# Kernel tuning notes

Measured on AMD Instinct MI355X. Metric: run time of the kernel, lower is better.

Reference implementation:

```python
import jax, jax.numpy as jnp
import numpy as np

S, B, NC = 16, 8, 5
D, H, DH = 256, 16, 16
PS, IMG = 7, 28
P = (IMG // PS) ** 2  # 16 patches
L = 2
PD = PS * PS * 1  # 49
EF, EFT = 4, 0.5
DFT = int(EFT * D)


def layernorm(x, g, b, eps=1e-5):
    m = x.mean(-1, keepdims=True)
    v = ((x - m) ** 2).mean(-1, keepdims=True)
    return (x - m) / jnp.sqrt(v + eps) * g + b


def patchify(x):
    # 's b c (h p1) (w p2) -> s b (h w) (p1 p2 c)'
    s, bb, c, hh, ww = x.shape
    h, w = hh // PS, ww // PS
    x = x.reshape(s, bb, c, h, PS, w, PS)
    x = x.transpose(0, 1, 3, 5, 4, 6, 2)
    return x.reshape(s, bb, h * w, PS * PS * c)


def srwm(x, Wy, Wq, Wk, wb, ln_g, ln_b):
    # Stateful self-referential weight matrix layer (Irie et al. 2022).
    # x: (S, Bn, h*dh); Wy/Wq/Wk: (h, dh, dh); wb: (h, 4, dh)
    s, bn, dim = x.shape
    h, dh = Wy.shape[0], Wy.shape[1]
    xs = x.reshape(s, bn, h, dh)
    bc = lambda W: jnp.broadcast_to(W[None], (bn,) + W.shape)

    def step(carry, xt):
        Wy, Wq, Wk, wb = carry
        y = jnp.einsum('bhij,bhj->bhi', Wy, xt)
        q = jnp.einsum('bhij,bhj->bhi', Wq, xt)
        k = jnp.einsum('bhij,bhj->bhi', Wk, xt)
        beta = jax.nn.sigmoid(jnp.einsum('bhcj,bhj->bhc', wb, xt))  # (Bn,h,4)
        qs = jax.nn.softmax(q, -1)
        ks = jax.nn.softmax(k, -1)
        # old values retrieved with k, target values generated with q
        vy_k = jnp.einsum('bhij,bhj->bhi', Wy, ks)
        vq_k = jnp.einsum('bhij,bhj->bhi', Wq, ks)
        vk_k = jnp.einsum('bhij,bhj->bhi', Wk, ks)
        vb_k = jnp.einsum('bhcj,bhj->bhc', wb, ks)
        vy_q = jax.nn.softmax(jnp.einsum('bhij,bhj->bhi', Wy, qs), -1)
        vq_q = jnp.einsum('bhij,bhj->bhi', Wq, qs)
        vk_q = jnp.einsum('bhij,bhj->bhi', Wk, qs)
        vb_q = jnp.einsum('bhcj,bhj->bhc', wb, qs)
        upd = lambda d, bt: bt[..., None, None] * d[..., None] * ks[..., None, :]
        Wy = Wy + upd(vy_q - vy_k, beta[..., 0])
        Wq = Wq + upd(vq_q - vq_k, beta[..., 1])
        Wk = Wk + upd(vk_q - vk_k, beta[..., 2])
        wb = wb + beta[..., 3, None, None] * (vb_q - vb_k)[..., None] * ks[..., None, :]
        return (Wy, Wq, Wk, wb), y

    _, ys = jax.lax.scan(step, (bc(Wy), bc(Wq), bc(Wk), bc(wb)), xs)
    return layernorm(ys.reshape(s, bn, dim), ln_g, ln_b)


def setup_inputs():
    key = jax.random.key(0)
    ks = iter(jax.random.split(key, 64))
    n = lambda shape, sc: jax.random.normal(next(ks), shape, jnp.float32) * sc
    return dict(
        x=jax.random.normal(next(ks), (S, B, 1, IMG, IMG), jnp.float32),
        fb=jax.random.randint(next(ks), (S, B), 0, NC),
        in_W=n((PD + NC, D), (PD + NC) ** -0.5), in_b=jnp.zeros((D,)),
        tk_Wy=n((L, 1, P, P), P ** -0.5), tk_Wq=n((L, 1, P, P), 0.01 * P ** -0.5),
        tk_Wk=n((L, 1, P, P), P ** -0.5), tk_wb=n((L, 1, 4, P), P ** -0.5),
        tk_lng=jnp.ones((L, P)), tk_lnb=jnp.zeros((L, P)),
        tkm_g=jnp.ones((L, D)), tkm_b=jnp.zeros((L, D)),
        tkm_W1=n((L, P, EF * P), P ** -0.5), tkm_b1=jnp.zeros((L, EF * P)),
        tkm_W2=n((L, EF * P, P), (EF * P) ** -0.5), tkm_b2=jnp.zeros((L, P)),
        ch_Wy=n((L, H, DH, DH), DH ** -0.5), ch_Wq=n((L, H, DH, DH), 0.01 * DH ** -0.5),
        ch_Wk=n((L, H, DH, DH), DH ** -0.5), ch_wb=n((L, H, 4, DH), DH ** -0.5),
        ch_lng=jnp.ones((L, D)), ch_lnb=jnp.zeros((L, D)),
        chm_g=jnp.ones((L, D)), chm_b=jnp.zeros((L, D)),
        chm_W1=n((L, D, DFT), D ** -0.5), chm_b1=jnp.zeros((L, DFT)),
        chm_W2=n((L, DFT, D), DFT ** -0.5), chm_b2=jnp.zeros((L, D)),
        fln_g=jnp.ones((D,)), fln_b=jnp.zeros((D,)),
        o_Wy=n((H, DH, DH), DH ** -0.5), o_Wq=n((H, DH, DH), 0.01 * DH ** -0.5),
        o_Wk=n((H, DH, DH), DH ** -0.5), o_wb=n((H, 4, DH), DH ** -0.5),
        o_lng=jnp.ones((D,)), o_lnb=jnp.zeros((D,)),
        out_W=n((D, NC), D ** -0.5), out_b=jnp.zeros((NC,)),
    )


def reference(x, fb, in_W, in_b, tk_Wy, tk_Wq, tk_Wk, tk_wb, tk_lng, tk_lnb,
              tkm_g, tkm_b, tkm_W1, tkm_b1, tkm_W2, tkm_b2,
              ch_Wy, ch_Wq, ch_Wk, ch_wb, ch_lng, ch_lnb,
              chm_g, chm_b, chm_W1, chm_b1, chm_W2, chm_b2,
              fln_g, fln_b, o_Wy, o_Wq, o_Wk, o_wb, o_lng, o_lnb, out_W, out_b):
    xp = patchify(x)  # (S,B,P,PD)
    emb = jnp.broadcast_to(jax.nn.one_hot(fb, NC)[:, :, None, :], (S, B, P, NC))
    h = jnp.concatenate([xp, emb.astype(xp.dtype)], -1) @ in_W + in_b  # (S,B,P,D)
    for i in range(L):
        # token SRWM: features = patch axis, batch = B*D
        t = jnp.swapaxes(h, -2, -1).reshape(S, B * D, P)
        t = srwm(t, tk_Wy[i], tk_Wq[i], tk_Wk[i], tk_wb[i], tk_lng[i], tk_lnb[i])
        h = jnp.swapaxes(t.reshape(S, B, D, P), -2, -1)
        # token mixer (pre-norm residual, FFN over patch axis)
        hn = jnp.swapaxes(layernorm(h, tkm_g[i], tkm_b[i]), -2, -1)
        hn = jax.nn.gelu(hn @ tkm_W1[i] + tkm_b1[i]) @ tkm_W2[i] + tkm_b2[i]
        h = h + jnp.swapaxes(hn, -2, -1)
        # channel SRWM: features = hidden axis, batch = B*P
        c = srwm(h.reshape(S, B * P, D), ch_Wy[i], ch_Wq[i], ch_Wk[i], ch_wb[i], ch_lng[i], ch_lnb[i])
        h = c.reshape(S, B, P, D)
        # channel mixer
        hn = layernorm(h, chm_g[i], chm_b[i])
        h = h + (jax.nn.gelu(hn @ chm_W1[i] + chm_b1[i]) @ chm_W2[i] + chm_b2[i])
    h = layernorm(h, fln_g, fln_b).mean(-2)  # (S,B,D) mean over patches
    h = srwm(h, o_Wy, o_Wq, o_Wk, o_wb, o_lng, o_lnb)
    return h @ out_W + out_b  # (S,B,NC)
```

## Files before the change

### kernel.cpp

```cpp
#include <hip/hip_runtime.h>
#include <math.h>

constexpr int cS  = 16;
constexpr int cB  = 8;
constexpr int cNC = 5;
constexpr int cD  = 256;
constexpr int cP  = 16;
constexpr int cPD = 49;
#define LEPS 1e-5f

__device__ __forceinline__ float frcp(float x) { return __builtin_amdgcn_rcpf(x); }
__device__ __forceinline__ float sigm(float x) { return frcp(1.0f + __expf(-x)); }
__device__ __forceinline__ float gelu_t(float x) {
  const float z = 1.5957691216057308f * (x + 0.044715f * x * x * x);
  return x * frcp(1.0f + __expf(-z));
}

template<int CTRL>
__device__ __forceinline__ float dpp_mov(float v) {
  return __int_as_float(__builtin_amdgcn_update_dpp(
      0, __float_as_int(v), CTRL, 0xF, 0xF, true));
}
__device__ __forceinline__ float row_sum16(float v) {
  v += dpp_mov<0xB1>(v);
  v += dpp_mov<0x4E>(v);
  v += dpp_mov<0x124>(v);
  v += dpp_mov<0x128>(v);
  return v;
}
__device__ __forceinline__ float wave_sum64(float v) {
  v = row_sum16(v);
  v += __shfl_xor(v, 16, 64);
  v += __shfl_xor(v, 32, 64);
  return v;
}

__device__ __forceinline__ float dot16(const float (&w)[16],
    const float4 a, const float4 b, const float4 c, const float4 d) {
  float s0 = w[0]  * a.x; s0 += w[1]  * a.y; s0 += w[2]  * a.z; s0 += w[3]  * a.w;
  float s1 = w[4]  * b.x; s1 += w[5]  * b.y; s1 += w[6]  * b.z; s1 += w[7]  * b.w;
  float s2 = w[8]  * c.x; s2 += w[9]  * c.y; s2 += w[10] * c.z; s2 += w[11] * c.w;
  float s3 = w[12] * d.x; s3 += w[13] * d.y; s3 += w[14] * d.z; s3 += w[15] * d.w;
  return (s0 + s1) + (s2 + s3);
}

__device__ __forceinline__ float srwm_step(
    float xv, float (&wy)[16], float (&wq)[16], float (&wk)[16], float (&wbr)[16],
    float* gl, const int r) {
  gl[r] = xv;
  __builtin_amdgcn_wave_barrier();
  const float4* g4 = (const float4*)gl;
  const float4 xa = g4[0], xb = g4[1], xc = g4[2], xd = g4[3];
  const float y  = dot16(wy,  xa, xb, xc, xd);
  const float q  = dot16(wq,  xa, xb, xc, xd);
  const float k  = dot16(wk,  xa, xb, xc, xd);
  const float bt = dot16(wbr, xa, xb, xc, xd);
  const float bsig = sigm(bt);
  const float eq = __expf(q), ek = __expf(k);
  gl[16 + r] = eq;
  gl[32 + r] = ek;
  gl[48 + r] = bsig;
  __builtin_amdgcn_wave_barrier();
  const float4 qa = g4[4], qb = g4[5], qc = g4[6],  qd = g4[7];
  const float4 ka = g4[8], kb = g4[9], kc = g4[10], kd = g4[11];
  const float4 bs4 = g4[12];
  const float ay  = dot16(wy,  qa, qb, qc, qd);
  const float vqq = dot16(wq,  qa, qb, qc, qd);
  const float vkq = dot16(wk,  qa, qb, qc, qd);
  const float vbq = dot16(wbr, qa, qb, qc, qd);
  const float vyk = dot16(wy,  ka, kb, kc, kd);
  const float vqk = dot16(wq,  ka, kb, kc, kd);
  const float vkk = dot16(wk,  ka, kb, kc, kd);
  const float vbk = dot16(wbr, ka, kb, kc, kd);
  const float sq = ((qa.x + qa.y) + (qa.z + qa.w)) + ((qb.x + qb.y) + (qb.z + qb.w))
                 + ((qc.x + qc.y) + (qc.z + qc.w)) + ((qd.x + qd.y) + (qd.z + qd.w));
  const float sk = ((ka.x + ka.y) + (ka.z + ka.w)) + ((kb.x + kb.y) + (kb.z + kb.w))
                 + ((kc.x + kc.y) + (kc.z + kc.w)) + ((kd.x + kd.y) + (kd.z + kd.w));
  const float rq = frcp(sq);
  const float rk = frcp(sk);
  const float ea = __expf(ay * rq);
  const float vyq = ea * frcp(row_sum16(ea));
  const float cy = bs4.x * (vyq      - vyk * rk) * rk;
  const float cq = bs4.y * (vqq * rq - vqk * rk) * rk;
  const float ck = bs4.z * (vkq * rq - vkk * rk) * rk;
  const float cb = bs4.w * (vbq * rq - vbk * rk) * rk;
  const float ks[16] = {ka.x, ka.y, ka.z, ka.w, kb.x, kb.y, kb.z, kb.w,
                        kc.x, kc.y, kc.z, kc.w, kd.x, kd.y, kd.z, kd.w};
#pragma unroll
  for (int j = 0; j < 16; ++j) {
    wy[j] += cy * ks[j]; wq[j] += cq * ks[j]; wk[j] += ck * ks[j]; wbr[j] += cb * ks[j];
  }
  return y;
}

__global__ __launch_bounds__(256) void k_embed(const float* __restrict__ x,
                                               const int* __restrict__ fb,
                                               const float* __restrict__ inW,
                                               const float* __restrict__ inb,
                                               float* __restrict__ h) {
  const int blk = blockIdx.x;
  const int p  = blk & 15;
  const int sb = blk >> 4;
  const int ph = p >> 2, pw = p & 3;
  __shared__ float sx[cPD];
  const int t = threadIdx.x;
  if (t < cPD) {
    const int p1 = t / 7, p2 = t % 7;
    sx[t] = x[(size_t)sb * 784 + (ph * 7 + p1) * 28 + (pw * 7 + p2)];
  }
  __syncthreads();
  const int cls = fb[sb];
  float acc = inb[t] + inW[(size_t)(cPD + cls) * cD + t];
#pragma unroll
  for (int j = 0; j < cPD; ++j) acc += sx[j] * inW[(size_t)j * cD + t];
  h[((size_t)sb * cP + p) * cD + t] = acc;
}

__global__ __launch_bounds__(128) void k_tok_srwm(
    float* __restrict__ h, const float* __restrict__ Wy0, const float* __restrict__ Wq0,
    const float* __restrict__ Wk0, const float* __restrict__ wb0,
    const float* __restrict__ lng, const float* __restrict__ lnb) {
  const int t    = threadIdx.x;
  const int lane = t & 63;
  const int w    = t >> 6;
  const int r    = lane & 15;
  const int li   = lane >> 4;
  const int b    = blockIdx.x >> 5;
  const int d    = ((blockIdx.x & 31) << 3) + (w << 2) + li;
  __shared__ __align__(16) float gscr[8][64];
  float* gl = gscr[t >> 4];
  float wy[16], wq[16], wk[16], wbr[16];
#pragma unroll
  for (int j = 0; j < 16; ++j) {
    wy[j]  = Wy0[r * 16 + j];
    wq[j]  = Wq0[r * 16 + j];
    wk[j]  = Wk0[r * 16 + j];
    wbr[j] = wb0[(r & 3) * 16 + j];
  }
  const float gg = lng[r], bb = lnb[r];
  float xp[16];
#pragma unroll
  for (int s = 0; s < 16; ++s)
    xp[s] = h[((size_t)(s * cB + b) * cP + r) * cD + d];
  for (int s = 0; s < cS; ++s) {
    const float y = srwm_step(xp[s], wy, wq, wk, wbr, gl, r);
    const float s1 = row_sum16(y);
    const float s2 = row_sum16(y * y);
    const float m = s1 * 0.0625f;
    const float var = s2 * 0.0625f - m * m;
    h[((size_t)(s * cB + b) * cP + r) * cD + d] = (y - m) * rsqrtf(var + LEPS) * gg + bb;
  }
}

__global__ __launch_bounds__(256) void k_tok_mixer(
    float* __restrict__ h, const float* __restrict__ g, const float* __restrict__ bta,
    const float* __restrict__ W1, const float* __restrict__ b1,
    const float* __restrict__ W2, const float* __restrict__ b2) {
  const int sb = blockIdx.x;
  const int t = threadIdx.x;
  __shared__ float tile[16][256];
  __shared__ float W1s[16 * 64], W2s[64 * 16];
  __shared__ float mean_[16], rstd_[16];
  __shared__ float red[16][17], red2[16][17];
  const size_t base = (size_t)sb * cP * cD;
#pragma unroll
  for (int p = 0; p < 16; ++p) tile[p][t] = h[base + p * 256 + t];
  W1s[t] = W1[t]; W1s[t + 256] = W1[t + 256]; W1s[t + 512] = W1[t + 512]; W1s[t + 768] = W1[t + 768];
  W2s[t] = W2[t]; W2s[t + 256] = W2[t + 256]; W2s[t + 512] = W2[t + 512]; W2s[t + 768] = W2[t + 768];
  __syncthreads();
  const int p = t >> 4, l = t & 15;
  float ps = 0.f, ps2 = 0.f;
#pragma unroll
  for (int k = 0; k < 16; ++k) { const float v = tile[p][l + 16 * k]; ps += v; ps2 += v * v; }
  red[p][l] = ps; red2[p][l] = ps2;
  __syncthreads();
  if (t < 16) {
    float sm = 0.f, s2 = 0.f;
#pragma unroll
    for (int k = 0; k < 16; ++k) { sm += red[t][k]; s2 += red2[t][k]; }
    const float m = sm * (1.f / 256.f);
    mean_[t] = m;
    rstd_[t] = rsqrtf(s2 * (1.f / 256.f) - m * m + LEPS);
  }
  __syncthreads();
  const float gd = g[t], bd = bta[t];
  float v[16], out[16];
#pragma unroll
  for (int pp = 0; pp < 16; ++pp) {
    v[pp] = (tile[pp][t] - mean_[pp]) * rstd_[pp] * gd + bd;
    out[pp] = b2[pp];
  }
  for (int e = 0; e < 64; ++e) {
    float acc = b1[e];
#pragma unroll
    for (int pp = 0; pp < 16; ++pp) acc += v[pp] * W1s[pp * 64 + e];
    const float ge = gelu_t(acc);
#pragma unroll
    for (int pp = 0; pp < 16; ++pp) out[pp] += ge * W2s[e * 16 + pp];
  }
#pragma unroll
  for (int pp = 0; pp < 16; ++pp) h[base + pp * 256 + t] = tile[pp][t] + out[pp];
}

__global__ __launch_bounds__(128) void k_ch_scan(
    const float* __restrict__ h, float* __restrict__ y2,
    const float* __restrict__ Wy0, const float* __restrict__ Wq0,
    const float* __restrict__ Wk0, const float* __restrict__ wb0) {
  const int t  = threadIdx.x;
  const int hg = blockIdx.x & 1;
  const int bp = blockIdx.x >> 1;
  const int hh = (hg << 3) + (t >> 4);
  const int r  = t & 15;
  const int d  = (hg << 7) + t;
  __shared__ __align__(16) float gscr[8][64];
  float* gl = gscr[t >> 4];
  float wy[16], wq[16], wk[16], wbr[16];
#pragma unroll
  for (int j = 0; j < 16; ++j) {
    wy[j]  = Wy0[(hh * 16 + r) * 16 + j];
    wq[j]  = Wq0[(hh * 16 + r) * 16 + j];
    wk[j]  = Wk0[(hh * 16 + r) * 16 + j];
    wbr[j] = wb0[(hh * 4 + (r & 3)) * 16 + j];
  }
  float xp[16];
#pragma unroll
  for (int s = 0; s < 16; ++s)
    xp[s] = h[(size_t)(s * cB * cP + bp) * cD + d];
  for (int s = 0; s < cS; ++s)
    y2[(size_t)(s * cB * cP + bp) * cD + d] = srwm_step(xp[s], wy, wq, wk, wbr, gl, r);
}

__global__ __launch_bounds__(256) void k_ch_ln_mix(
    const float* __restrict__ y2, float* __restrict__ h,
    const float* __restrict__ lng, const float* __restrict__ lnb,
    const float* __restrict__ mg, const float* __restrict__ mb,
    const float* __restrict__ W1, const float* __restrict__ b1,
    const float* __restrict__ W2, const float* __restrict__ b2) {
  const int t = threadIdx.x;
  const int row0 = blockIdx.x * 8;
  __shared__ float yv[8][256];
  __shared__ float lnv[8][256];
  __shared__ float hid[8][128];
  const float4* yp4 = (const float4*)(y2 + (size_t)row0 * cD);
  ((float4*)yv)[t]       = yp4[t];
  ((float4*)yv)[t + 256] = yp4[t + 256];
  __syncthreads();
  const int r32 = t >> 5, l = t & 31;
  const float4 eg0 = ((const float4*)lng)[l * 2];
  const float4 eg1 = ((const float4*)lng)[l * 2 + 1];
  const float4 eb0 = ((const float4*)lnb)[l * 2];
  const float4 eb1 = ((const float4*)lnb)[l * 2 + 1];
  const float4 mg0 = ((const float4*)mg)[l * 2];
  const float4 mg1 = ((const float4*)mg)[l * 2 + 1];
  const float4 mb0 = ((const float4*)mb)[l * 2];
  const float4 mb1 = ((const float4*)mb)[l * 2 + 1];
  const float4 y0 = ((const float4*)yv[r32])[l * 2];
  const float4 y1 = ((const float4*)yv[r32])[l * 2 + 1];
  float s1 = y0.x + y0.y + y0.z + y0.w + y1.x + y1.y + y1.z + y1.w;
  float s2 = y0.x * y0.x + y0.y * y0.y + y0.z * y0.z + y0.w * y0.w +
             y1.x * y1.x + y1.y * y1.y + y1.z * y1.z + y1.w * y1.w;
#pragma unroll
  for (int o = 1; o < 32; o <<= 1) {
    s1 += __shfl_xor(s1, o, 32);
    s2 += __shfl_xor(s2, o, 32);
  }
  const float m1 = s1 * (1.f / 256.f);
  const float rst1 = rsqrtf(s2 * (1.f / 256.f) - m1 * m1 + LEPS);
  float4 a0, a1;
  a0.x = (y0.x - m1) * rst1 * eg0.x + eb0.x; a0.y = (y0.y - m1) * rst1 * eg0.y + eb0.y;
  a0.z = (y0.z - m1) * rst1 * eg0.z + eb0.z; a0.w = (y0.w - m1) * rst1 * eg0.w + eb0.w;
  a1.x = (y1.x - m1) * rst1 * eg1.x + eb1.x; a1.y = (y1.y - m1) * rst1 * eg1.y + eb1.y;
  a1.z = (y1.z - m1) * rst1 * eg1.z + eb1.z; a1.w = (y1.w - m1) * rst1 * eg1.w + eb1.w;
  float u1 = a0.x + a0.y + a0.z + a0.w + a1.x + a1.y + a1.z + a1.w;
  float u2 = a0.x * a0.x + a0.y * a0.y + a0.z * a0.z + a0.w * a0.w +
             a1.x * a1.x + a1.y * a1.y + a1.z * a1.z + a1.w * a1.w;
#pragma unroll
  for (int o = 1; o < 32; o <<= 1) {
    u1 += __shfl_xor(u1, o, 32);
    u2 += __shfl_xor(u2, o, 32);
  }
  const float m2 = u1 * (1.f / 256.f);
  const float rst2 = rsqrtf(u2 * (1.f / 256.f) - m2 * m2 + LEPS);
  float4 L0, L1;
  L0.x = (a0.x - m2) * rst2 * mg0.x + mb0.x; L0.y = (a0.y - m2) * rst2 * mg0.y + mb0.y;
  L0.z = (a0.z - m2) * rst2 * mg0.z + mb0.z; L0.w = (a0.w - m2) * rst2 * mg0.w + mb0.w;
  L1.x = (a1.x - m2) * rst2 * mg1.x + mb1.x; L1.y = (a1.y - m2) * rst2 * mg1.y + mb1.y;
  L1.z = (a1.z - m2) * rst2 * mg1.z + mb1.z; L1.w = (a1.w - m2) * rst2 * mg1.w + mb1.w;
  ((float4*)lnv[r32])[l * 2]     = L0;
  ((float4*)lnv[r32])[l * 2 + 1] = L1;
  __syncthreads();
  {
    const float4* W1f = (const float4*)W1;
    float4 acc = ((const float4*)b1)[l];
    for (int j = 0; j < 256; ++j) {
      const float xj = lnv[r32][j];
      const float4 wv = W1f[j * 32 + l];
      acc.x += xj * wv.x; acc.y += xj * wv.y; acc.z += xj * wv.z; acc.w += xj * wv.w;
    }
    float4 hv;
    hv.x = gelu_t(acc.x); hv.y = gelu_t(acc.y);
    hv.z = gelu_t(acc.z); hv.w = gelu_t(acc.w);
    ((float4*)hid[r32])[l] = hv;
  }
  __syncthreads();
  {
    const float4* W2f = (const float4*)W2;
    float4 o0 = ((const float4*)b2)[l * 2];
    float4 o1 = ((const float4*)b2)[l * 2 + 1];
    for (int e = 0; e < 128; ++e) {
      const float xh = hid[r32][e];
      const float4 w0 = W2f[e * 64 + l * 2];
      const float4 w1 = W2f[e * 64 + l * 2 + 1];
      o0.x += xh * w0.x; o0.y += xh * w0.y; o0.z += xh * w0.z; o0.w += xh * w0.w;
      o1.x += xh * w1.x; o1.y += xh * w1.y; o1.z += xh * w1.z; o1.w += xh * w1.w;
    }
    o0.x += a0.x; o0.y += a0.y; o0.z += a0.z; o0.w += a0.w;
    o1.x += a1.x; o1.y += a1.y; o1.z += a1.z; o1.w += a1.w;
    float4* op = (float4*)(h + ((size_t)row0 + r32) * cD);
    op[l * 2]     = o0;
    op[l * 2 + 1] = o1;
  }
}

__global__ __launch_bounds__(256) void k_fln_mean(
    const float* __restrict__ h, const float* __restrict__ gg, const float* __restrict__ bbv,
    float* __restrict__ o) {
  const int sb = blockIdx.x;
  const int t = threadIdx.x;
  const int lane = t & 63, w = t >> 6;
  const float4 g4 = ((const float4*)gg)[lane];
  const float4 b4 = ((const float4*)bbv)[lane];
  float a0 = 0.f, a1 = 0.f, a2 = 0.f, a3 = 0.f;
  for (int pp = 0; pp < 4; ++pp) {
    const int p = w * 4 + pp;
    const float4 v4 = ((const float4*)(h + ((size_t)sb * cP + p) * cD))[lane];
    const float s1 = wave_sum64(v4.x + v4.y + v4.z + v4.w);
    const float s2 = wave_sum64(v4.x * v4.x + v4.y * v4.y + v4.z * v4.z + v4.w * v4.w);
    const float m = s1 * (1.f / 256.f);
    const float rst = rsqrtf(s2 * (1.f / 256.f) - m * m + LEPS);
    a0 += (v4.x - m) * rst * g4.x + b4.x;
    a1 += (v4.y - m) * rst * g4.y + b4.y;
    a2 += (v4.z - m) * rst * g4.z + b4.z;
    a3 += (v4.w - m) * rst * g4.w + b4.w;
  }
  __shared__ float sacc[4][256];
  float4* sp = (float4*)sacc[w];
  sp[lane] = make_float4(a0, a1, a2, a3);
  __syncthreads();
  o[(size_t)sb * cD + t] = (sacc[0][t] + sacc[1][t] + sacc[2][t] + sacc[3][t]) * (1.f / 16.f);
}

__global__ __launch_bounds__(256, 1) void k_out_srwm(
    const float* __restrict__ gin, float* __restrict__ outp,
    const float* __restrict__ Wy0, const float* __restrict__ Wq0,
    const float* __restrict__ Wk0, const float* __restrict__ wb0,
    const float* __restrict__ lng, const float* __restrict__ lnb,
    const float* __restrict__ outW, const float* __restrict__ outb) {
  const int t = threadIdx.x;
  const int lane = t & 63;
  const int w = t >> 6;
  const int hh = t >> 4, r = t & 15;
  const int b = blockIdx.x;
  __shared__ float ymat[16][256];
  __shared__ float gwm[cNC][256];
  __shared__ float GBp[4][10];
  __shared__ float GBs[10];
  __shared__ __align__(16) float gscr[16][64];
  float* gl = gscr[hh];
  float wy[16], wq[16], wk[16], wbr[16];
#pragma unroll
  for (int j = 0; j < 16; ++j) {
    wy[j]  = Wy0[(hh * 16 + r) * 16 + j];
    wq[j]  = Wq0[(hh * 16 + r) * 16 + j];
    wk[j]  = Wk0[(hh * 16 + r) * 16 + j];
    wbr[j] = wb0[(hh * 4 + (r & 3)) * 16 + j];
  }
  {
    const float gg = lng[t], bbl = lnb[t];
    float pg[cNC], pbv[cNC];
#pragma unroll
    for (int c = 0; c < cNC; ++c) {
      const float wv = outW[(size_t)t * cNC + c];
      const float gwv = gg * wv;
      gwm[c][t] = gwv;
      pg[c] = wave_sum64(gwv);
      pbv[c] = wave_sum64(bbl * wv);
    }
    if (lane == 0) {
#pragma unroll
      for (int c = 0; c < cNC; ++c) { GBp[w][c] = pg[c]; GBp[w][5 + c] = pbv[c]; }
    }
    __syncthreads();
    if (t < 10) GBs[t] = GBp[0][t] + GBp[1][t] + GBp[2][t] + GBp[3][t];
    __syncthreads();
  }
  float xp[16];
#pragma unroll
  for (int s = 0; s < 16; ++s) xp[s] = gin[(size_t)(s * cB + b) * cD + t];
  for (int s = 0; s < cS; ++s)
    ymat[s][t] = srwm_step(xp[s], wy, wq, wk, wbr, gl, r);
  __syncthreads();
  for (int k2 = 0; k2 < 4; ++k2) {
    const int sidx = w * 4 + k2;
    const float4 y4 = ((const float4*)ymat[sidx])[lane];
    const float s1 = wave_sum64(y4.x + y4.y + y4.z + y4.w);
    const float s2 = wave_sum64(y4.x * y4.x + y4.y * y4.y + y4.z * y4.z + y4.w * y4.w);
    float S[cNC];
#pragma unroll
    for (int c = 0; c < cNC; ++c) {
      const float4 g4 = ((const float4*)gwm[c])[lane];
      S[c] = wave_sum64(y4.x * g4.x + y4.y * g4.y + y4.z * g4.z + y4.w * g4.w);
    }
    if (lane == 0) {
      const float m = s1 * (1.f / 256.f);
      const float var = s2 * (1.f / 256.f) - m * m;
      const float rst = rsqrtf(var + LEPS);
#pragma unroll
      for (int c = 0; c < cNC; ++c) {
        outp[(size_t)(sidx * cB + b) * cNC + c] =
            outb[c] + rst * S[c] - rst * m * GBs[c] + GBs[5 + c];
      }
    }
  }
}

extern "C" void kernel_launch(void* const* d_in, const int* in_sizes, int n_in,
                              void* d_out, int out_size, void* d_ws, size_t ws_size,
                              hipStream_t stream) {
  const float* x     = (const float*)d_in[0];
  const int*   fb    = (const int*)d_in[1];
  const float* inW   = (const float*)d_in[2];
  const float* inb   = (const float*)d_in[3];
  const float* tkWy  = (const float*)d_in[4];
  const float* tkWq  = (const float*)d_in[5];
  const float* tkWk  = (const float*)d_in[6];
  const float* tkwb  = (const float*)d_in[7];
  const float* tklng = (const float*)d_in[8];
  const float* tklnb = (const float*)d_in[9];
  const float* tkmg  = (const float*)d_in[10];
  const float* tkmb  = (const float*)d_in[11];
  const float* tkmW1 = (const float*)d_in[12];
  const float* tkmb1 = (const float*)d_in[13];
  const float* tkmW2 = (const float*)d_in[14];
  const float* tkmb2 = (const float*)d_in[15];
  const float* chWy  = (const float*)d_in[16];
  const float* chWq  = (const float*)d_in[17];
  const float* chWk  = (const float*)d_in[18];
  const float* chwb  = (const float*)d_in[19];
  const float* chlng = (const float*)d_in[20];
  const float* chlnb = (const float*)d_in[21];
  const float* chmg  = (const float*)d_in[22];
  const float* chmb  = (const float*)d_in[23];
  const float* chmW1 = (const float*)d_in[24];
  const float* chmb1 = (const float*)d_in[25];
  const float* chmW2 = (const float*)d_in[26];
  const float* chmb2 = (const float*)d_in[27];
  const float* flng  = (const float*)d_in[28];
  const float* flnb  = (const float*)d_in[29];
  const float* oWy   = (const float*)d_in[30];
  const float* oWq   = (const float*)d_in[31];
  const float* oWk   = (const float*)d_in[32];
  const float* owb   = (const float*)d_in[33];
  const float* olng  = (const float*)d_in[34];
  const float* olnb  = (const float*)d_in[35];
  const float* outW  = (const float*)d_in[36];
  const float* outb  = (const float*)d_in[37];

  float* h    = (float*)d_ws;
  float* gbuf = h + (size_t)cS * cB * cP * cD;
  float* y2   = gbuf + (size_t)cS * cB * cD;
  float* outp = (float*)d_out;

  k_embed<<<dim3(cS * cB * cP), dim3(256), 0, stream>>>(x, fb, inW, inb, h);
  for (int i = 0; i < 2; ++i) {
    k_tok_srwm<<<dim3(256), dim3(128), 0, stream>>>(
        h, tkWy + i * 256, tkWq + i * 256, tkWk + i * 256, tkwb + i * 64,
        tklng + i * 16, tklnb + i * 16);
    k_tok_mixer<<<dim3(cS * cB), dim3(256), 0, stream>>>(
        h, tkmg + i * 256, tkmb + i * 256, tkmW1 + i * 1024, tkmb1 + i * 64,
        tkmW2 + i * 1024, tkmb2 + i * 16);
    k_ch_scan<<<dim3(cB * cP * 2), dim3(128), 0, stream>>>(
        h, y2, chWy + i * 4096, chWq + i * 4096, chWk + i * 4096, chwb + i * 1024);
    k_ch_ln_mix<<<dim3(cS * cB * cP / 8), dim3(256), 0, stream>>>(
        y2, h, chlng + i * 256, chlnb + i * 256,
        chmg + i * 256, chmb + i * 256, chmW1 + i * 32768, chmb1 + i * 128,
        chmW2 + i * 32768, chmb2 + i * 256);
  }
  k_fln_mean<<<dim3(cS * cB), dim3(256), 0, stream>>>(h, flng, flnb, gbuf);
  k_out_srwm<<<dim3(cB), dim3(256), 0, stream>>>(
      gbuf, outp, oWy, oWq, oWk, owb, olng, olnb, outW, outb);
}
```

Before: 300.4 us.

## Fuse all stages into one persistent kernel with software grid barriers

Replaces the sequence of about ten kernel launches with a single persistent kernel of 256 blocks that runs every stage and separates them with a sense-reversing atomic grid barrier. The embed stage is also reorganised so each block computes eight patches from the full image held in shared memory. The aim is to remove per-launch overhead and inter-kernel gaps, since each stage is small. In exchange, the SRWM stages now leave half the threads idle in 256-thread blocks, several stages use only a subset of blocks, and correctness depends on all 256 blocks being co-resident.

```diff
diff --git a/kernel.cpp b/kernel.cpp
--- a/kernel.cpp
+++ b/kernel.cpp
@@ -8,6 +8,10 @@
 constexpr int cP  = 16;
 constexpr int cPD = 49;
 #define LEPS 1e-5f
+#define NBLK 256
+
+__device__ unsigned g_cnt[2];
+__device__ unsigned g_sense;
 
 __device__ __forceinline__ float frcp(float x) { return __builtin_amdgcn_rcpf(x); }
 __device__ __forceinline__ float sigm(float x) { return frcp(1.0f + __expf(-x)); }
@@ -93,332 +97,397 @@
   return y;
 }
 
-__global__ __launch_bounds__(256) void k_embed(const float* __restrict__ x,
-                                               const int* __restrict__ fb,
-                                               const float* __restrict__ inW,
-                                               const float* __restrict__ inb,
-                                               float* __restrict__ h) {
-  const int blk = blockIdx.x;
-  const int p  = blk & 15;
-  const int sb = blk >> 4;
-  const int ph = p >> 2, pw = p & 3;
-  __shared__ float sx[cPD];
+struct SM_M {
+  float tile[16][256];
+  float W1s[1024]; float W2s[1024];
+  float mean_[16]; float rstd_[16];
+  float red[16][17]; float red2[16][17];
+};
+struct SM_X { float yv[8][256]; float lnv[8][256]; float hid[8][128]; };
+struct SM_O {
+  float ymat[16][256]; float gwm[cNC][256];
+  float GBp[4][10]; float GBs[10]; float gscr[16][64];
+};
+union SMem {
+  float sx[784];
+  float gscr[8][64];
+  SM_M m;
+  SM_X x;
+  float sacc[4][256];
+  SM_O o;
+};
+
+struct Args {
+  const float* x; const int* fb; const float* inW; const float* inb;
+  const float *tkWy, *tkWq, *tkWk, *tkwb, *tklng, *tklnb;
+  const float *tkmg, *tkmb, *tkmW1, *tkmb1, *tkmW2, *tkmb2;
+  const float *chWy, *chWq, *chWk, *chwb, *chlng, *chlnb;
+  const float *chmg, *chmb, *chmW1, *chmb1, *chmW2, *chmb2;
+  const float *flng, *flnb;
+  const float *oWy, *oWq, *oWk, *owb, *olng, *olnb, *outW, *outb;
+  float *h, *gbuf, *y2, *outp;
+};
+
+#define GSYNC()                                                                \
+  do {                                                                         \
+    __syncthreads();                                                           \
+    ++kbar;                                                                    \
+    if (t == 0) {                                                              \
+      __threadfence();                                                         \
+      const unsigned tgt = kbar & 1u;                                          \
+      const unsigned old = __hip_atomic_fetch_add(                             \
+          &g_cnt[kbar & 1u], 1u, __ATOMIC_ACQ_REL, __HIP_MEMORY_SCOPE_AGENT);  \
+      if (old == (unsigned)(NBLK - 1)) {                                       \
+        __hip_atomic_store(&g_cnt[kbar & 1u], 0u, __ATOMIC_RELAXED,            \
+                           __HIP_MEMORY_SCOPE_AGENT);                          \
+        __hip_atomic_store(&g_sense, tgt, __ATOMIC_RELEASE,                    \
+                           __HIP_MEMORY_SCOPE_AGENT);                          \
+      } else {                                                                 \
+        while (__hip_atomic_load(&g_sense, __ATOMIC_ACQUIRE,                   \
+                                 __HIP_MEMORY_SCOPE_AGENT) != tgt)             \
+          __builtin_amdgcn_s_sleep(16);                                        \
+      }                                                                        \
+    }                                                                          \
+    __syncthreads();                                                           \
+  } while (0)
+
+__global__ __launch_bounds__(256, 1) void k_mega(Args a) {
   const int t = threadIdx.x;
-  if (t < cPD) {
-    const int p1 = t / 7, p2 = t % 7;
-    sx[t] = x[(size_t)sb * 784 + (ph * 7 + p1) * 28 + (pw * 7 + p2)];
+  const int bid = blockIdx.x;
+  __shared__ __align__(16) SMem sm;
+  unsigned kbar = 0;
+
+  {
+    const int sb = bid >> 1, h2 = bid & 1;
+    for (int i = t; i < 784; i += 256) sm.sx[i] = a.x[(size_t)sb * 784 + i];
+    __syncthreads();
+    const int cls = a.fb[sb];
+    const int d = t;
+    float acc[8];
+    const float base0 = a.inb[d] + a.inW[(size_t)(cPD + cls) * cD + d];
+#pragma unroll
+    for (int p8 = 0; p8 < 8; ++p8) acc[p8] = base0;
+    for (int p1 = 0; p1 < 7; ++p1) {
+      for (int p2 = 0; p2 < 7; ++p2) {
+        const float wj = a.inW[(size_t)(p1 * 7 + p2) * cD + d];
+        const int jo = p1 * 28 + p2;
+#pragma unroll
+        for (int p8 = 0; p8 < 8; ++p8) {
+          const int p = h2 * 8 + p8;
+          acc[p8] += wj * sm.sx[(p >> 2) * 196 + (p & 3) * 7 + jo];
+        }
+      }
+    }
+#pragma unroll
+    for (int p8 = 0; p8 < 8; ++p8)
+      a.h[((size_t)sb * cP + h2 * 8 + p8) * cD + d] = acc[p8];
   }
-  __syncthreads();
-  const int cls = fb[sb];
-  float acc = inb[t] + inW[(size_t)(cPD + cls) * cD + t];
-#pragma unroll
-  for (int j = 0; j < cPD; ++j) acc += sx[j] * inW[(size_t)j * cD + t];
-  h[((size_t)sb * cP + p) * cD + t] = acc;
-}
-
-__global__ __launch_bounds__(128) void k_tok_srwm(
-    float* __restrict__ h, const float* __restrict__ Wy0, const float* __restrict__ Wq0,
-    const float* __restrict__ Wk0, const float* __restrict__ wb0,
-    const float* __restrict__ lng, const float* __restrict__ lnb) {
-  const int t    = threadIdx.x;
-  const int lane = t & 63;
-  const int w    = t >> 6;
-  const int r    = lane & 15;
-  const int li   = lane >> 4;
-  const int b    = blockIdx.x >> 5;
-  const int d    = ((blockIdx.x & 31) << 3) + (w << 2) + li;
-  __shared__ __align__(16) float gscr[8][64];
-  float* gl = gscr[t >> 4];
-  float wy[16], wq[16], wk[16], wbr[16];
-#pragma unroll
-  for (int j = 0; j < 16; ++j) {
-    wy[j]  = Wy0[r * 16 + j];
-    wq[j]  = Wq0[r * 16 + j];
-    wk[j]  = Wk0[r * 16 + j];
-    wbr[j] = wb0[(r & 3) * 16 + j];
+  GSYNC();
+
+  for (int i = 0; i < 2; ++i) {
+    {
+      const float* Wy0 = a.tkWy + i * 256;
+      const float* Wq0 = a.tkWq + i * 256;
+      const float* Wk0 = a.tkWk + i * 256;
+      const float* wb0 = a.tkwb + i * 64;
+      const float* lng = a.tklng + i * 16;
+      const float* lnb = a.tklnb + i * 16;
+      if (t < 128) {
+        const int lane = t & 63;
+        const int w    = t >> 6;
+        const int r    = lane & 15;
+        const int li   = lane >> 4;
+        const int b    = bid >> 5;
+        const int d    = ((bid & 31) << 3) + (w << 2) + li;
+        float* gl = sm.gscr[t >> 4];
+        float wy[16], wq[16], wk[16], wbr[16];
+#pragma unroll
+        for (int j = 0; j < 16; ++j) {
+          wy[j]  = Wy0[r * 16 + j];
+          wq[j]  = Wq0[r * 16 + j];
+          wk[j]  = Wk0[r * 16 + j];
+          wbr[j] = wb0[(r & 3) * 16 + j];
+        }
+        const float gg = lng[r], bb = lnb[r];
+        float xp[16];
+#pragma unroll
+        for (int s = 0; s < 16; ++s)
+          xp[s] = a.h[((size_t)(s * cB + b) * cP + r) * cD + d];
+        for (int s = 0; s < cS; ++s) {
+          const float y = srwm_step(xp[s], wy, wq, wk, wbr, gl, r);
+          const float s1 = row_sum16(y);
+          const float s2 = row_sum16(y * y);
+          const float m = s1 * 0.0625f;
+          const float var = s2 * 0.0625f - m * m;
+          a.h[((size_t)(s * cB + b) * cP + r) * cD + d] =
+              (y - m) * rsqrtf(var + LEPS) * gg + bb;
+        }
+      }
+    }
+    GSYNC();
+
+    if (bid < 128) {
+      const float* g   = a.tkmg + i * 256;
+      const float* bta = a.tkmb + i * 256;
+      const float* W1  = a.tkmW1 + i * 1024;
+      const float* b1  = a.tkmb1 + i * 64;
+      const float* W2  = a.tkmW2 + i * 1024;
+      const float* b2  = a.tkmb2 + i * 16;
+      const size_t base = (size_t)bid * cP * cD;
+#pragma unroll
+      for (int p = 0; p < 16; ++p) sm.m.tile[p][t] = a.h[base + p * 256 + t];
+      sm.m.W1s[t] = W1[t]; sm.m.W1s[t + 256] = W1[t + 256];
+      sm.m.W1s[t + 512] = W1[t + 512]; sm.m.W1s[t + 768] = W1[t + 768];
+      sm.m.W2s[t] = W2[t]; sm.m.W2s[t + 256] = W2[t + 256];
+      sm.m.W2s[t + 512] = W2[t + 512]; sm.m.W2s[t + 768] = W2[t + 768];
+      __syncthreads();
+      const int p = t >> 4, l = t & 15;
+      float ps = 0.f, ps2 = 0.f;
+#pragma unroll
+      for (int k = 0; k < 16; ++k) {
+        const float v = sm.m.tile[p][l + 16 * k]; ps += v; ps2 += v * v;
+      }
+      sm.m.red[p][l] = ps; sm.m.red2[p][l] = ps2;
+      __syncthreads();
+      if (t < 16) {
+        float smv = 0.f, s2 = 0.f;
+#pragma unroll
+        for (int k = 0; k < 16; ++k) { smv += sm.m.red[t][k]; s2 += sm.m.red2[t][k]; }
+        const float m = smv * (1.f / 256.f);
+        sm.m.mean_[t] = m;
+        sm.m.rstd_[t] = rsqrtf(s2 * (1.f / 256.f) - m * m + LEPS);
+      }
+      __syncthreads();
+      const float gd = g[t], bd = bta[t];
+      float v[16], out[16];
+#pragma unroll
+      for (int pp = 0; pp < 16; ++pp) {
+        v[pp] = (sm.m.tile[pp][t] - sm.m.mean_[pp]) * sm.m.rstd_[pp] * gd + bd;
+        out[pp] = b2[pp];
+      }
+      for (int e = 0; e < 64; ++e) {
+        float acc = b1[e];
+#pragma unroll
+        for (int pp = 0; pp < 16; ++pp) acc += v[pp] * sm.m.W1s[pp * 64 + e];
+        const float ge = gelu_t(acc);
+#pragma unroll
+        for (int pp = 0; pp < 16; ++pp) out[pp] += ge * sm.m.W2s[e * 16 + pp];
+      }
+#pragma unroll
+      for (int pp = 0; pp < 16; ++pp)
+        a.h[base + pp * 256 + t] = sm.m.tile[pp][t] + out[pp];
+    }
+    GSYNC();
+
+    {
+      const float* Wy0 = a.chWy + i * 4096;
+      const float* Wq0 = a.chWq + i * 4096;
+      const float* Wk0 = a.chWk + i * 4096;
+      const float* wb0 = a.chwb + i * 1024;
+      if (t < 128) {
+        const int hg = bid & 1;
+        const int bp = bid >> 1;
+        const int hh = (hg << 3) + (t >> 4);
+        const int r  = t & 15;
+        const int d  = (hg << 7) + t;
+        float* gl = sm.gscr[t >> 4];
+        float wy[16], wq[16], wk[16], wbr[16];
+#pragma unroll
+        for (int j = 0; j < 16; ++j) {
+          wy[j]  = Wy0[(hh * 16 + r) * 16 + j];
+          wq[j]  = Wq0[(hh * 16 + r) * 16 + j];
+          wk[j]  = Wk0[(hh * 16 + r) * 16 + j];
+          wbr[j] = wb0[(hh * 4 + (r & 3)) * 16 + j];
+        }
+        float xp[16];
+#pragma unroll
+        for (int s = 0; s < 16; ++s)
+          xp[s] = a.h[(size_t)(s * cB * cP + bp) * cD + d];
+        for (int s = 0; s < cS; ++s)
+          a.y2[(size_t)(s * cB * cP + bp) * cD + d] =
+              srwm_step(xp[s], wy, wq, wk, wbr, gl, r);
+      }
+    }
+    GSYNC();
+
+    {
+      const float* lng = a.chlng + i * 256;
+      const float* lnb = a.chlnb + i * 256;
+      const float* mg  = a.chmg + i * 256;
+      const float* mb  = a.chmb + i * 256;
+      const float* W1  = a.chmW1 + i * 32768;
+      const float* b1  = a.chmb1 + i * 128;
+      const float* W2  = a.chmW2 + i * 32768;
+      const float* b2  = a.chmb2 + i * 256;
+      const int row0 = bid * 8;
+      const float4* yp4 = (const float4*)(a.y2 + (size_t)row0 * cD);
+      ((float4*)sm.x.yv)[t]       = yp4[t];
+      ((float4*)sm.x.yv)[t + 256] = yp4[t + 256];
+      __syncthreads();
+      const int r32 = t >> 5, l = t & 31;
+      const float4 eg0 = ((const float4*)lng)[l * 2];
+      const float4 eg1 = ((const float4*)lng)[l * 2 + 1];
+      const float4 eb0 = ((const float4*)lnb)[l * 2];
+      const float4 eb1 = ((const float4*)lnb)[l * 2 + 1];
+      const float4 mg0 = ((const float4*)mg)[l * 2];
+      const float4 mg1 = ((const float4*)mg)[l * 2 + 1];
+      const float4 mb0 = ((const float4*)mb)[l * 2];
+      const float4 mb1 = ((const float4*)mb)[l * 2 + 1];
+      const float4 y0 = ((const float4*)sm.x.yv[r32])[l * 2];
+      const float4 y1 = ((const float4*)sm.x.yv[r32])[l * 2 + 1];
+      float s1 = y0.x + y0.y + y0.z + y0.w + y1.x + y1.y + y1.z + y1.w;
+      float s2 = y0.x * y0.x + y0.y * y0.y + y0.z * y0.z + y0.w * y0.w +
+                 y1.x * y1.x + y1.y * y1.y + y1.z * y1.z + y1.w * y1.w;
+#pragma unroll
+      for (int o = 1; o < 32; o <<= 1) {
+        s1 += __shfl_xor(s1, o, 32);
+        s2 += __shfl_xor(s2, o, 32);
+      }
+      const float m1 = s1 * (1.f / 256.f);
+      const float rst1 = rsqrtf(s2 * (1.f / 256.f) - m1 * m1 + LEPS);
+      float4 a0, a1;
+      a0.x = (y0.x - m1) * rst1 * eg0.x + eb0.x; a0.y = (y0.y - m1) * rst1 * eg0.y + eb0.y;
+      a0.z = (y0.z - m1) * rst1 * eg0.z + eb0.z; a0.w = (y0.w - m1) * rst1 * eg0.w + eb0.w;
+      a1.x = (y1.x - m1) * rst1 * eg1.x + eb1.x; a1.y = (y1.y - m1) * rst1 * eg1.y + eb1.y;
+      a1.z = (y1.z - m1) * rst1 * eg1.z + eb1.z; a1.w = (y1.w - m1) * rst1 * eg1.w + eb1.w;
+      float u1 = a0.x + a0.y + a0.z + a0.w + a1.x + a1.y + a1.z + a1.w;
+      float u2 = a0.x * a0.x + a0.y * a0.y + a0.z * a0.z + a0.w * a0.w +
+                 a1.x * a1.x + a1.y * a1.y + a1.z * a1.z + a1.w * a1.w;
+#pragma unroll
+      for (int o = 1; o < 32; o <<= 1) {
+        u1 += __shfl_xor(u1, o, 32);
+        u2 += __shfl_xor(u2, o, 32);
+      }
+      const float m2 = u1 * (1.f / 256.f);
+      const float rst2 = rsqrtf(u2 * (1.f / 256.f) - m2 * m2 + LEPS);
+      float4 L0, L1;
+      L0.x = (a0.x - m2) * rst2 * mg0.x + mb0.x; L0.y = (a0.y - m2) * rst2 * mg0.y + mb0.y;
+      L0.z = (a0.z - m2) * rst2 * mg0.z + mb0.z; L0.w = (a0.w - m2) * rst2 * mg0.w + mb0.w;
+      L1.x = (a1.x - m2) * rst2 * mg1.x + mb1.x; L1.y = (a1.y - m2) * rst2 * mg1.y + mb1.y;
+      L1.z = (a1.z - m2) * rst2 * mg1.z + mb1.z; L1.w = (a1.w - m2) * rst2 * mg1.w + mb1.w;
+      ((float4*)sm.x.lnv[r32])[l * 2]     = L0;
+      ((float4*)sm.x.lnv[r32])[l * 2 + 1] = L1;
+      __syncthreads();
+      {
+        const float4* W1f = (const float4*)W1;
+        float4 acc = ((const float4*)b1)[l];
+        for (int j = 0; j < 256; ++j) {
+          const float xj = sm.x.lnv[r32][j];
+          const float4 wv = W1f[j * 32 + l];
+          acc.x += xj * wv.x; acc.y += xj * wv.y; acc.z += xj * wv.z; acc.w += xj * wv.w;
+        }
+        float4 hv;
+        hv.x = gelu_t(acc.x); hv.y = gelu_t(acc.y);
+        hv.z = gelu_t(acc.z); hv.w = gelu_t(acc.w);
+        ((float4*)sm.x.hid[r32])[l] = hv;
+      }
+      __syncthreads();
+      {
+        const float4* W2f = (const float4*)W2;
+        float4 o0 = ((const float4*)b2)[l * 2];
+        float4 o1 = ((const float4*)b2)[l * 2 + 1];
+        for (int e = 0; e < 128; ++e) {
+          const float xh = sm.x.hid[r32][e];
+          const float4 w0 = W2f[e * 64 + l * 2];
+          const float4 w1 = W2f[e * 64 + l * 2 + 1];
+          o0.x += xh * w0.x; o0.y += xh * w0.y; o0.z += xh * w0.z; o0.w += xh * w0.w;
+          o1.x += xh * w1.x; o1.y += xh * w1.y; o1.z += xh * w1.z; o1.w += xh * w1.w;
+        }
+        o0.x += a0.x; o0.y += a0.y; o0.z += a0.z; o0.w += a0.w;
+        o1.x += a1.x; o1.y += a1.y; o1.z += a1.z; o1.w += a1.w;
+        float4* op = (float4*)(a.h + ((size_t)row0 + r32) * cD);
+        op[l * 2]     = o0;
+        op[l * 2 + 1] = o1;
+      }
+    }
+    GSYNC();
   }
-  const float gg = lng[r], bb = lnb[r];
-  float xp[16];
-#pragma unroll
-  for (int s = 0; s < 16; ++s)
-    xp[s] = h[((size_t)(s * cB + b) * cP + r) * cD + d];
-  for (int s = 0; s < cS; ++s) {
-    const float y = srwm_step(xp[s], wy, wq, wk, wbr, gl, r);
-    const float s1 = row_sum16(y);
-    const float s2 = row_sum16(y * y);
-    const float m = s1 * 0.0625f;
-    const float var = s2 * 0.0625f - m * m;
-    h[((size_t)(s * cB + b) * cP + r) * cD + d] = (y - m) * rsqrtf(var + LEPS) * gg + bb;
+
+  if (bid < 128) {
+    const int sb = bid;
+    const int lane = t & 63, w = t >> 6;
+    const float4 g4 = ((const float4*)a.flng)[lane];
+    const float4 b4 = ((const float4*)a.flnb)[lane];
+    float a0 = 0.f, a1 = 0.f, a2 = 0.f, a3 = 0.f;
+    for (int pp = 0; pp < 4; ++pp) {
+      const int p = w * 4 + pp;
+      const float4 v4 = ((const float4*)(a.h + ((size_t)sb * cP + p) * cD))[lane];
+      const float s1 = wave_sum64(v4.x + v4.y + v4.z + v4.w);
+      const float s2 = wave_sum64(v4.x * v4.x + v4.y * v4.y + v4.z * v4.z + v4.w * v4.w);
+      const float m = s1 * (1.f / 256.f);
+      const float rst = rsqrtf(s2 * (1.f / 256.f) - m * m + LEPS);
+      a0 += (v4.x - m) * rst * g4.x + b4.x;
+      a1 += (v4.y - m) * rst * g4.y + b4.y;
+      a2 += (v4.z - m) * rst * g4.z + b4.z;
+      a3 += (v4.w - m) * rst * g4.w + b4.w;
+    }
+    float4* sp = (float4*)sm.sacc[w];
+    sp[lane] = make_float4(a0, a1, a2, a3);
+    __syncthreads();
+    a.gbuf[(size_t)sb * cD + t] =
+        (sm.sacc[0][t] + sm.sacc[1][t] + sm.sacc[2][t] + sm.sacc[3][t]) * (1.f / 16.f);
   }
-}
-
-__global__ __launch_bounds__(256) void k_tok_mixer(
-    float* __restrict__ h, const float* __restrict__ g, const float* __restrict__ bta,
-    const float* __restrict__ W1, const float* __restrict__ b1,
-    const float* __restrict__ W2, const float* __restrict__ b2) {
-  const int sb = blockIdx.x;
-  const int t = threadIdx.x;
-  __shared__ float tile[16][256];
-  __shared__ float W1s[16 * 64], W2s[64 * 16];
-  __shared__ float mean_[16], rstd_[16];
-  __shared__ float red[16][17], red2[16][17];
-  const size_t base = (size_t)sb * cP * cD;
-#pragma unroll
-  for (int p = 0; p < 16; ++p) tile[p][t] = h[base + p * 256 + t];
-  W1s[t] = W1[t]; W1s[t + 256] = W1[t + 256]; W1s[t + 512] = W1[t + 512]; W1s[t + 768] = W1[t + 768];
-  W2s[t] = W2[t]; W2s[t + 256] = W2[t + 256]; W2s[t + 512] = W2[t + 512]; W2s[t + 768] = W2[t + 768];
-  __syncthreads();
-  const int p = t >> 4, l = t & 15;
-  float ps = 0.f, ps2 = 0.f;
-#pragma unroll
-  for (int k = 0; k < 16; ++k) { const float v = tile[p][l + 16 * k]; ps += v; ps2 += v * v; }
-  red[p][l] = ps; red2[p][l] = ps2;
-  __syncthreads();
-  if (t < 16) {
-    float sm = 0.f, s2 = 0.f;
-#pragma unroll
-    for (int k = 0; k < 16; ++k) { sm += red[t][k]; s2 += red2[t][k]; }
-    const float m = sm * (1.f / 256.f);
-    mean_[t] = m;
-    rstd_[t] = rsqrtf(s2 * (1.f / 256.f) - m * m + LEPS);
-  }
-  __syncthreads();
-  const float gd = g[t], bd = bta[t];
-  float v[16], out[16];
-#pragma unroll
-  for (int pp = 0; pp < 16; ++pp) {
-    v[pp] = (tile[pp][t] - mean_[pp]) * rstd_[pp] * gd + bd;
-    out[pp] = b2[pp];
-  }
-  for (int e = 0; e < 64; ++e) {
-    float acc = b1[e];
-#pragma unroll
-    for (int pp = 0; pp < 16; ++pp) acc += v[pp] * W1s[pp * 64 + e];
-    const float ge = gelu_t(acc);
-#pragma unroll
-    for (int pp = 0; pp < 16; ++pp) out[pp] += ge * W2s[e * 16 + pp];
-  }
-#pragma unroll
-  for (int pp = 0; pp < 16; ++pp) h[base + pp * 256 + t] = tile[pp][t] + out[pp];
-}
-
-__global__ __launch_bounds__(128) void k_ch_scan(
-    const float* __restrict__ h, float* __restrict__ y2,
-    const float* __restrict__ Wy0, const float* __restrict__ Wq0,
-    const float* __restrict__ Wk0, const float* __restrict__ wb0) {
-  const int t  = threadIdx.x;
-  const int hg = blockIdx.x & 1;
-  const int bp = blockIdx.x >> 1;
-  const int hh = (hg << 3) + (t >> 4);
-  const int r  = t & 15;
-  const int d  = (hg << 7) + t;
-  __shared__ __align__(16) float gscr[8][64];
-  float* gl = gscr[t >> 4];
-  float wy[16], wq[16], wk[16], wbr[16];
-#pragma unroll
-  for (int j = 0; j < 16; ++j) {
-    wy[j]  = Wy0[(hh * 16 + r) * 16 + j];
-    wq[j]  = Wq0[(hh * 16 + r) * 16 + j];
-    wk[j]  = Wk0[(hh * 16 + r) * 16 + j];
-    wbr[j] = wb0[(hh * 4 + (r & 3)) * 16 + j];
-  }
-  float xp[16];
-#pragma unroll
-  for (int s = 0; s < 16; ++s)
-    xp[s] = h[(size_t)(s * cB * cP + bp) * cD + d];
-  for (int s = 0; s < cS; ++s)
-    y2[(size_t)(s * cB * cP + bp) * cD + d] = srwm_step(xp[s], wy, wq, wk, wbr, gl, r);
-}
-
-__global__ __launch_bounds__(256) void k_ch_ln_mix(
-    const float* __restrict__ y2, float* __restrict__ h,
-    const float* __restrict__ lng, const float* __restrict__ lnb,
-    const float* __restrict__ mg, const float* __restrict__ mb,
-    const float* __restrict__ W1, const float* __restrict__ b1,
-    const float* __restrict__ W2, const float* __restrict__ b2) {
-  const int t = threadIdx.x;
-  const int row0 = blockIdx.x * 8;
-  __shared__ float yv[8][256];
-  __shared__ float lnv[8][256];
-  __shared__ float hid[8][128];
-  const float4* yp4 = (const float4*)(y2 + (size_t)row0 * cD);
-  ((float4*)yv)[t]       = yp4[t];
-  ((float4*)yv)[t + 256] = yp4[t + 256];
-  __syncthreads();
-  const int r32 = t >> 5, l = t & 31;
-  const float4 eg0 = ((const float4*)lng)[l * 2];
-  const float4 eg1 = ((const float4*)lng)[l * 2 + 1];
-  const float4 eb0 = ((const float4*)lnb)[l * 2];
-  const float4 eb1 = ((const float4*)lnb)[l * 2 + 1];
-  const float4 mg0 = ((const float4*)mg)[l * 2];
-  const float4 mg1 = ((const float4*)mg)[l * 2 + 1];
-  const float4 mb0 = ((const float4*)mb)[l * 2];
-  const float4 mb1 = ((const float4*)mb)[l * 2 + 1];
-  const float4 y0 = ((const float4*)yv[r32])[l * 2];
-  const float4 y1 = ((const float4*)yv[r32])[l * 2 + 1];
-  float s1 = y0.x + y0.y + y0.z + y0.w + y1.x + y1.y + y1.z + y1.w;
-  float s2 = y0.x * y0.x + y0.y * y0.y + y0.z * y0.z + y0.w * y0.w +
-             y1.x * y1.x + y1.y * y1.y + y1.z * y1.z + y1.w * y1.w;
-#pragma unroll
-  for (int o = 1; o < 32; o <<= 1) {
-    s1 += __shfl_xor(s1, o, 32);
-    s2 += __shfl_xor(s2, o, 32);
-  }
-  const float m1 = s1 * (1.f / 256.f);
-  const float rst1 = rsqrtf(s2 * (1.f / 256.f) - m1 * m1 + LEPS);
-  float4 a0, a1;
-  a0.x = (y0.x - m1) * rst1 * eg0.x + eb0.x; a0.y = (y0.y - m1) * rst1 * eg0.y + eb0.y;
-  a0.z = (y0.z - m1) * rst1 * eg0.z + eb0.z; a0.w = (y0.w - m1) * rst1 * eg0.w + eb0.w;
-  a1.x = (y1.x - m1) * rst1 * eg1.x + eb1.x; a1.y = (y1.y - m1) * rst1 * eg1.y + eb1.y;
-  a1.z = (y1.z - m1) * rst1 * eg1.z + eb1.z; a1.w = (y1.w - m1) * rst1 * eg1.w + eb1.w;
-  float u1 = a0.x + a0.y + a0.z + a0.w + a1.x + a1.y + a1.z + a1.w;
-  float u2 = a0.x * a0.x + a0.y * a0.y + a0.z * a0.z + a0.w * a0.w +
-             a1.x * a1.x + a1.y * a1.y + a1.z * a1.z + a1.w * a1.w;
-#pragma unroll
-  for (int o = 1; o < 32; o <<= 1) {
-    u1 += __shfl_xor(u1, o, 32);
-    u2 += __shfl_xor(u2, o, 32);
-  }
-  const float m2 = u1 * (1.f / 256.f);
-  const float rst2 = rsqrtf(u2 * (1.f / 256.f) - m2 * m2 + LEPS);
-  float4 L0, L1;
-  L0.x = (a0.x - m2) * rst2 * mg0.x + mb0.x; L0.y = (a0.y - m2) * rst2 * mg0.y + mb0.y;
-  L0.z = (a0.z - m2) * rst2 * mg0.z + mb0.z; L0.w = (a0.w - m2) * rst2 * mg0.w + mb0.w;
-  L1.x = (a1.x - m2) * rst2 * mg1.x + mb1.x; L1.y = (a1.y - m2) * rst2 * mg1.y + mb1.y;
-  L1.z = (a1.z - m2) * rst2 * mg1.z + mb1.z; L1.w = (a1.w - m2) * rst2 * mg1.w + mb1.w;
-  ((float4*)lnv[r32])[l * 2]     = L0;
-  ((float4*)lnv[r32])[l * 2 + 1] = L1;
-  __syncthreads();
-  {
-    const float4* W1f = (const float4*)W1;
-    float4 acc = ((const float4*)b1)[l];
-    for (int j = 0; j < 256; ++j) {
-      const float xj = lnv[r32][j];
-      const float4 wv = W1f[j * 32 + l];
-      acc.x += xj * wv.x; acc.y += xj * wv.y; acc.z += xj * wv.z; acc.w += xj * wv.w;
-    }
-    float4 hv;
-    hv.x = gelu_t(acc.x); hv.y = gelu_t(acc.y);
-    hv.z = gelu_t(acc.z); hv.w = gelu_t(acc.w);
-    ((float4*)hid[r32])[l] = hv;
-  }
-  __syncthreads();
-  {
-    const float4* W2f = (const float4*)W2;
-    float4 o0 = ((const float4*)b2)[l * 2];
-    float4 o1 = ((const float4*)b2)[l * 2 + 1];
-    for (int e = 0; e < 128; ++e) {
-      const float xh = hid[r32][e];
-      const float4 w0 = W2f[e * 64 + l * 2];
-      const float4 w1 = W2f[e * 64 + l * 2 + 1];
-      o0.x += xh * w0.x; o0.y += xh * w0.y; o0.z += xh * w0.z; o0.w += xh * w0.w;
-      o1.x += xh * w1.x; o1.y += xh * w1.y; o1.z += xh * w1.z; o1.w += xh * w1.w;
-    }
-    o0.x += a0.x; o0.y += a0.y; o0.z += a0.z; o0.w += a0.w;
-    o1.x += a1.x; o1.y += a1.y; o1.z += a1.z; o1.w += a1.w;
-    float4* op = (float4*)(h + ((size_t)row0 + r32) * cD);
-    op[l * 2]     = o0;
-    op[l * 2 + 1] = o1;
-  }
-}
-
-__global__ __launch_bounds__(256) void k_fln_mean(
-    const float* __restrict__ h, const float* __restrict__ gg, const float* __restrict__ bbv,
-    float* __restrict__ o) {
-  const int sb = blockIdx.x;
-  const int t = threadIdx.x;
-  const int lane = t & 63, w = t >> 6;
-  const float4 g4 = ((const float4*)gg)[lane];
-  const float4 b4 = ((const float4*)bbv)[lane];
-  float a0 = 0.f, a1 = 0.f, a2 = 0.f, a3 = 0.f;
-  for (int pp = 0; pp < 4; ++pp) {
-    const int p = w * 4 + pp;
-    const float4 v4 = ((const float4*)(h + ((size_t)sb * cP + p) * cD))[lane];
-    const float s1 = wave_sum64(v4.x + v4.y + v4.z + v4.w);
-    const float s2 = wave_sum64(v4.x * v4.x + v4.y * v4.y + v4.z * v4.z + v4.w * v4.w);
-    const float m = s1 * (1.f / 256.f);
-    const float rst = rsqrtf(s2 * (1.f / 256.f) - m * m + LEPS);
-    a0 += (v4.x - m) * rst * g4.x + b4.x;
-    a1 += (v4.y - m) * rst * g4.y + b4.y;
-    a2 += (v4.z - m) * rst * g4.z + b4.z;
-    a3 += (v4.w - m) * rst * g4.w + b4.w;
-  }
-  __shared__ float sacc[4][256];
-  float4* sp = (float4*)sacc[w];
-  sp[lane] = make_float4(a0, a1, a2, a3);
-  __syncthreads();
-  o[(size_t)sb * cD + t] = (sacc[0][t] + sacc[1][t] + sacc[2][t] + sacc[3][t]) * (1.f / 16.f);
-}
-
-__global__ __launch_bounds__(256, 1) void k_out_srwm(
-    const float* __restrict__ gin, float* __restrict__ outp,
-    const float* __restrict__ Wy0, const float* __restrict__ Wq0,
-    const float* __restrict__ Wk0, const float* __restrict__ wb0,
-    const float* __restrict__ lng, const float* __restrict__ lnb,
-    const float* __restrict__ outW, const float* __restrict__ outb) {
-  const int t = threadIdx.x;
-  const int lane = t & 63;
-  const int w = t >> 6;
-  const int hh = t >> 4, r = t & 15;
-  const int b = blockIdx.x;
-  __shared__ float ymat[16][256];
-  __shared__ float gwm[cNC][256];
-  __shared__ float GBp[4][10];
-  __shared__ float GBs[10];
-  __shared__ __align__(16) float gscr[16][64];
-  float* gl = gscr[hh];
-  float wy[16], wq[16], wk[16], wbr[16];
-#pragma unroll
-  for (int j = 0; j < 16; ++j) {
-    wy[j]  = Wy0[(hh * 16 + r) * 16 + j];
-    wq[j]  = Wq0[(hh * 16 + r) * 16 + j];
-    wk[j]  = Wk0[(hh * 16 + r) * 16 + j];
-    wbr[j] = wb0[(hh * 4 + (r & 3)) * 16 + j];
-  }
-  {
-    const float gg = lng[t], bbl = lnb[t];
-    float pg[cNC], pbv[cNC];
-#pragma unroll
-    for (int c = 0; c < cNC; ++c) {
-      const float wv = outW[(size_t)t * cNC + c];
-      const float gwv = gg * wv;
-      gwm[c][t] = gwv;
-      pg[c] = wave_sum64(gwv);
-      pbv[c] = wave_sum64(bbl * wv);
-    }
-    if (lane == 0) {
-#pragma unroll
-      for (int c = 0; c < cNC; ++c) { GBp[w][c] = pg[c]; GBp[w][5 + c] = pbv[c]; }
-    }
+  GSYNC();
+
+  if (bid < 8) {
+    const int lane = t & 63;
+    const int w = t >> 6;
+    const int hh = t >> 4, r = t & 15;
+    const int b = bid;
+    float* gl = sm.o.gscr[hh];
+    float wy[16], wq[16], wk[16], wbr[16];
+#pragma unroll
+    for (int j = 0; j < 16; ++j) {
+      wy[j]  = a.oWy[(hh * 16 + r) * 16 + j];
+      wq[j]  = a.oWq[(hh * 16 + r) * 16 + j];
+      wk[j]  = a.oWk[(hh * 16 + r) * 16 + j];
+      wbr[j] = a.owb[(hh * 4 + (r & 3)) * 16 + j];
+    }
+    {
+      const float gg = a.olng[t], bbl = a.olnb[t];
+      float pg[cNC], pbv[cNC];
+#pragma unroll
+      for (int c = 0; c < cNC; ++c) {
+        const float wv = a.outW[(size_t)t * cNC + c];
+        const float gwv = gg * wv;
+        sm.o.gwm[c][t] = gwv;
+        pg[c] = wave_sum64(gwv);
+        pbv[c] = wave_sum64(bbl * wv);
+      }
+      if (lane == 0) {
+#pragma unroll
+        for (int c = 0; c < cNC; ++c) { sm.o.GBp[w][c] = pg[c]; sm.o.GBp[w][5 + c] = pbv[c]; }
+      }
+      __syncthreads();
+      if (t < 10) sm.o.GBs[t] = sm.o.GBp[0][t] + sm.o.GBp[1][t] + sm.o.GBp[2][t] + sm.o.GBp[3][t];
+      __syncthreads();
+    }
+    float xp[16];
+#pragma unroll
+    for (int s = 0; s < 16; ++s) xp[s] = a.gbuf[(size_t)(s * cB + b) * cD + t];
+    for (int s = 0; s < cS; ++s)
+      sm.o.ymat[s][t] = srwm_step(xp[s], wy, wq, wk, wbr, gl, r);
     __syncthreads();
-    if (t < 10) GBs[t] = GBp[0][t] + GBp[1][t] + GBp[2][t] + GBp[3][t];
-    __syncthreads();
-  }
-  float xp[16];
-#pragma unroll
-  for (int s = 0; s < 16; ++s) xp[s] = gin[(size_t)(s * cB + b) * cD + t];
-  for (int s = 0; s < cS; ++s)
-    ymat[s][t] = srwm_step(xp[s], wy, wq, wk, wbr, gl, r);
-  __syncthreads();
-  for (int k2 = 0; k2 < 4; ++k2) {
-    const int sidx = w * 4 + k2;
-    const float4 y4 = ((const float4*)ymat[sidx])[lane];
-    const float s1 = wave_sum64(y4.x + y4.y + y4.z + y4.w);
-    const float s2 = wave_sum64(y4.x * y4.x + y4.y * y4.y + y4.z * y4.z + y4.w * y4.w);
-    float S[cNC];
-#pragma unroll
-    for (int c = 0; c < cNC; ++c) {
-      const float4 g4 = ((const float4*)gwm[c])[lane];
-      S[c] = wave_sum64(y4.x * g4.x + y4.y * g4.y + y4.z * g4.z + y4.w * g4.w);
-    }
-    if (lane == 0) {
-      const float m = s1 * (1.f / 256.f);
-      const float var = s2 * (1.f / 256.f) - m * m;
-      const float rst = rsqrtf(var + LEPS);
+    for (int k2 = 0; k2 < 4; ++k2) {
+      const int sidx = w * 4 + k2;
+      const float4 y4 = ((const float4*)sm.o.ymat[sidx])[lane];
+      const float s1 = wave_sum64(y4.x + y4.y + y4.z + y4.w);
+      const float s2 = wave_sum64(y4.x * y4.x + y4.y * y4.y + y4.z * y4.z + y4.w * y4.w);
+      float S[cNC];
 #pragma unroll
       for (int c = 0; c < cNC; ++c) {
-        outp[(size_t)(sidx * cB + b) * cNC + c] =
-            outb[c] + rst * S[c] - rst * m * GBs[c] + GBs[5 + c];
+        const float4 g4 = ((const float4*)sm.o.gwm[c])[lane];
+        S[c] = wave_sum64(y4.x * g4.x + y4.y * g4.y + y4.z * g4.z + y4.w * g4.w);
+      }
+      if (lane == 0) {
+        const float m = s1 * (1.f / 256.f);
+        const float var = s2 * (1.f / 256.f) - m * m;
+        const float rst = rsqrtf(var + LEPS);
+#pragma unroll
+        for (int c = 0; c < cNC; ++c) {
+          a.outp[(size_t)(sidx * cB + b) * cNC + c] =
+              a.outb[c] + rst * S[c] - rst * m * sm.o.GBs[c] + sm.o.GBs[5 + c];
+        }
       }
     }
   }
@@ -427,66 +496,50 @@
 extern "C" void kernel_launch(void* const* d_in, const int* in_sizes, int n_in,
                               void* d_out, int out_size, void* d_ws, size_t ws_size,
                               hipStream_t stream) {
-  const float* x     = (const float*)d_in[0];
-  const int*   fb    = (const int*)d_in[1];
-  const float* inW   = (const float*)d_in[2];
-  const float* inb   = (const float*)d_in[3];
-  const float* tkWy  = (const float*)d_in[4];
-  const float* tkWq  = (const float*)d_in[5];
-  const float* tkWk  = (const float*)d_in[6];
-  const float* tkwb  = (const float*)d_in[7];
-  const float* tklng = (const float*)d_in[8];
-  const float* tklnb = (const float*)d_in[9];
-  const float* tkmg  = (const float*)d_in[10];
-  const float* tkmb  = (const float*)d_in[11];
-  const float* tkmW1 = (const float*)d_in[12];
-  const float* tkmb1 = (const float*)d_in[13];
-  const float* tkmW2 = (const float*)d_in[14];
-  const float* tkmb2 = (const float*)d_in[15];
-  const float* chWy  = (const float*)d_in[16];
-  const float* chWq  = (const float*)d_in[17];
-  const float* chWk  = (const float*)d_in[18];
-  const float* chwb  = (const float*)d_in[19];
-  const float* chlng = (const float*)d_in[20];
-  const float* chlnb = (const float*)d_in[21];
-  const float* chmg  = (const float*)d_in[22];
-  const float* chmb  = (const float*)d_in[23];
-  const float* chmW1 = (const float*)d_in[24];
-  const float* chmb1 = (const float*)d_in[25];
-  const float* chmW2 = (const float*)d_in[26];
-  const float* chmb2 = (const float*)d_in[27];
-  const float* flng  = (const float*)d_in[28];
-  const float* flnb  = (const float*)d_in[29];
-  const float* oWy   = (const float*)d_in[30];
-  const float* oWq   = (const float*)d_in[31];
-  const float* oWk   = (const float*)d_in[32];
-  const float* owb   = (const float*)d_in[33];
-  const float* olng  = (const float*)d_in[34];
-  const float* olnb  = (const float*)d_in[35];
-  const float* outW  = (const float*)d_in[36];
-  const float* outb  = (const float*)d_in[37];
-
-  float* h    = (float*)d_ws;
-  float* gbuf = h + (size_t)cS * cB * cP * cD;
-  float* y2   = gbuf + (size_t)cS * cB * cD;
-  float* outp = (float*)d_out;
-
-  k_embed<<<dim3(cS * cB * cP), dim3(256), 0, stream>>>(x, fb, inW, inb, h);
-  for (int i = 0; i < 2; ++i) {
-    k_tok_srwm<<<dim3(256), dim3(128), 0, stream>>>(
-        h, tkWy + i * 256, tkWq + i * 256, tkWk + i * 256, tkwb + i * 64,
-        tklng + i * 16, tklnb + i * 16);
-    k_tok_mixer<<<dim3(cS * cB), dim3(256), 0, stream>>>(
-        h, tkmg + i * 256, tkmb + i * 256, tkmW1 + i * 1024, tkmb1 + i * 64,
-        tkmW2 + i * 1024, tkmb2 + i * 16);
-    k_ch_scan<<<dim3(cB * cP * 2), dim3(128), 0, stream>>>(
-        h, y2, chWy + i * 4096, chWq + i * 4096, chWk + i * 4096, chwb + i * 1024);
-    k_ch_ln_mix<<<dim3(cS * cB * cP / 8), dim3(256), 0, stream>>>(
-        y2, h, chlng + i * 256, chlnb + i * 256,
-        chmg + i * 256, chmb + i * 256, chmW1 + i * 32768, chmb1 + i * 128,
-        chmW2 + i * 32768, chmb2 + i * 256);
-  }
-  k_fln_mean<<<dim3(cS * cB), dim3(256), 0, stream>>>(h, flng, flnb, gbuf);
-  k_out_srwm<<<dim3(cB), dim3(256), 0, stream>>>(
-      gbuf, outp, oWy, oWq, oWk, owb, olng, olnb, outW, outb);
-}
+  Args a;
+  a.x     = (const float*)d_in[0];
+  a.fb    = (const int*)d_in[1];
+  a.inW   = (const float*)d_in[2];
+  a.inb   = (const float*)d_in[3];
+  a.tkWy  = (const float*)d_in[4];
+  a.tkWq  = (const float*)d_in[5];
+  a.tkWk  = (const float*)d_in[6];
+  a.tkwb  = (const float*)d_in[7];
+  a.tklng = (const float*)d_in[8];
+  a.tklnb = (const float*)d_in[9];
+  a.tkmg  = (const float*)d_in[10];
+  a.tkmb  = (const float*)d_in[11];
+  a.tkmW1 = (const float*)d_in[12];
+  a.tkmb1 = (const float*)d_in[13];
+  a.tkmW2 = (const float*)d_in[14];
+  a.tkmb2 = (const float*)d_in[15];
+  a.chWy  = (const float*)d_in[16];
+  a.chWq  = (const float*)d_in[17];
+  a.chWk  = (const float*)d_in[18];
+  a.chwb  = (const float*)d_in[19];
+  a.chlng = (const float*)d_in[20];
+  a.chlnb = (const float*)d_in[21];
+  a.chmg  = (const float*)d_in[22];
+  a.chmb  = (const float*)d_in[23];
+  a.chmW1 = (const float*)d_in[24];
+  a.chmb1 = (const float*)d_in[25];
+  a.chmW2 = (const float*)d_in[26];
+  a.chmb2 = (const float*)d_in[27];
+  a.flng  = (const float*)d_in[28];
+  a.flnb  = (const float*)d_in[29];
+  a.oWy   = (const float*)d_in[30];
+  a.oWq   = (const float*)d_in[31];
+  a.oWk   = (const float*)d_in[32];
+  a.owb   = (const float*)d_in[33];
+  a.olng  = (const float*)d_in[34];
+  a.olnb  = (const float*)d_in[35];
+  a.outW  = (const float*)d_in[36];
+  a.outb  = (const float*)d_in[37];
+
+  a.h    = (float*)d_ws;
+  a.gbuf = a.h + (size_t)cS * cB * cP * cD;
+  a.y2   = a.gbuf + (size_t)cS * cB * cD;
+  a.outp = (float*)d_out;
+
+  k_mega<<<dim3(NBLK), dim3(256), 0, stream>>>(a);
+}
```

After: 606.1 us. 102% more time.
